# Kernel tuning notes

Hardware: AMD Instinct MI355X
Metric: run time of the kernel (lower is better)

## Reference

```python
import jax, jax.numpy as jnp
import numpy as np

HID = 257

def _lstm_cell(x, h, c, wih, whh, bih, bhh):
    # PyTorch gate order: i, f, g, o
    g = wih @ x + bih + whh @ h + bhh
    i, f, gg, o = jnp.split(g, 4)
    c2 = jax.nn.sigmoid(f) * c + jax.nn.sigmoid(i) * jnp.tanh(gg)
    h2 = jax.nn.sigmoid(o) * jnp.tanh(c2)
    return h2, c2

def _bilstm(x, state, p):
    # seq_len==1 bidirectional LSTM: fwd and bwd cells both see the single step
    hf, cf, hb, cb = state
    hf2, cf2 = _lstm_cell(x, hf, cf, p[0], p[1], p[2], p[3])
    hb2, cb2 = _lstm_cell(x, hb, cb, p[4], p[5], p[6], p[7])
    return jnp.concatenate([hf2, hb2]), (hf2, cf2, hb2, cb2)

def _conv_relu(x, w, b):
    y = jax.lax.conv_general_dilated(x, w, (1, 1), 'VALID', dimension_numbers=('NCHW', 'OIHW', 'NCHW'))
    return jax.nn.relu(y + b[None, :, None, None])

def _forward(src, conv1_w, conv1_b, conv2_w, conv2_b, conv3_w, conv3_b, conv4_w, conv4_b,
             conv5_w, conv5_b, conv6_w, conv6_b, fc1_w, fc1_b, fc2_w, fc2_b, fc3_w, fc3_b,
             enc_wih_f, enc_whh_f, enc_bih_f, enc_bhh_f, enc_wih_b, enc_whh_b, enc_bih_b, enc_bhh_b,
             dec_wih_f, dec_whh_f, dec_bih_f, dec_bhh_f, dec_wih_b, dec_whh_b, dec_bih_b, dec_bhh_b,
             lin_w, lin_b, maxlinelen):
    # AdaptiveMaxPool2d(32) on 128x128 == 4x4/stride-4 max pool
    x = src.reshape(1, 32, 32, 4, 32, 4).max(axis=(3, 5))
    x = _conv_relu(x, conv1_w, conv1_b)   # (1,64,30,30)
    x = _conv_relu(x, conv2_w, conv2_b)   # (1,128,28,28)
    x = _conv_relu(x, conv3_w, conv3_b)   # (1,256,26,26)
    x = _conv_relu(x, conv4_w, conv4_b)   # (1,512,24,24)
    x = _conv_relu(x, conv5_w, conv5_b)   # (1,512,22,22)
    x = _conv_relu(x, conv6_w, conv6_b)   # (1,512,21,21) (k=2)
    # AdaptiveMaxPool2d(10) on 21x21 == window-3/stride-2 max pool
    x = jax.lax.reduce_window(x, -jnp.inf, jax.lax.max, (1, 1, 3, 3), (1, 1, 2, 2), 'VALID')
    x = x.reshape(-1)                     # (51200,)
    x = jax.nn.relu(fc1_w @ x + fc1_b)
    x = jax.nn.relu(fc2_w @ x + fc2_b)
    feat = fc3_w @ x + fc3_b              # (128,)
    enc_p = (enc_wih_f, enc_whh_f, enc_bih_f, enc_bhh_f, enc_wih_b, enc_whh_b, enc_bih_b, enc_bhh_b)
    dec_p = (dec_wih_f, dec_whh_f, dec_bih_f, dec_bhh_f, dec_wih_b, dec_whh_b, dec_bih_b, dec_bhh_b)
    z = jnp.zeros((HID,), src.dtype)
    y, enc_state = _bilstm(feat, (z, z, z, z), enc_p)  # encode, zero init state
    x = lin_w @ y + lin_b
    y, state = _bilstm(x, enc_state, dec_p)            # decode seeded with encode hidden
    x = lin_w @ y + lin_b                              # out[0]
    def step(carry, _):
        xc, st = carry
        yy, st2 = _bilstm(xc, st, dec_p)
        x2 = lin_w @ yy + lin_b
        return (x2, st2), x2
    _, rest = jax.lax.scan(step, (x, state), None, length=maxlinelen - 1)
    return jnp.concatenate([x[None, :], rest], axis=0)  # (maxlinelen, 257)

def setup_inputs():
    key = jax.random.key(0)
    ks = iter(jax.random.split(key, 64))
    def W(shape, fan):
        return jax.random.normal(next(ks), shape, jnp.float32) / np.float32(np.sqrt(fan))
    d = {}
    d['src'] = jax.random.normal(next(ks), (1, 32, 128, 128), jnp.float32)
    convs = [(64, 32, 3), (128, 64, 3), (256, 128, 3), (512, 256, 3), (512, 512, 3), (512, 512, 2)]
    for i, (o, c, k) in enumerate(convs, 1):
        d['conv%d_w' % i] = W((o, c, k, k), c * k * k)
        d['conv%d_b' % i] = jnp.zeros((o,), jnp.float32)
    d['fc1_w'] = W((2048, 51200), 51200); d['fc1_b'] = jnp.zeros((2048,), jnp.float32)
    d['fc2_w'] = W((512, 2048), 2048);    d['fc2_b'] = jnp.zeros((512,), jnp.float32)
    d['fc3_w'] = W((128, 512), 512);      d['fc3_b'] = jnp.zeros((128,), jnp.float32)
    for pre, nin in (('enc', 128), ('dec', HID)):
        for dr in ('f', 'b'):
            d['%s_wih_%s' % (pre, dr)] = W((4 * HID, nin), HID)
            d['%s_whh_%s' % (pre, dr)] = W((4 * HID, HID), HID)
            d['%s_bih_%s' % (pre, dr)] = jnp.zeros((4 * HID,), jnp.float32)
            d['%s_bhh_%s' % (pre, dr)] = jnp.zeros((4 * HID,), jnp.float32)
    d['lin_w'] = W((HID, 2 * HID), 2 * HID)
    d['lin_b'] = jnp.zeros((HID,), jnp.float32)
    d['maxlinelen'] = 128
    return d

def reference(src, conv1_w, conv1_b, conv2_w, conv2_b, conv3_w, conv3_b, conv4_w, conv4_b,
              conv5_w, conv5_b, conv6_w, conv6_b, fc1_w, fc1_b, fc2_w, fc2_b, fc3_w, fc3_b,
              enc_wih_f, enc_whh_f, enc_bih_f, enc_bhh_f, enc_wih_b, enc_whh_b, enc_bih_b, enc_bhh_b,
              dec_wih_f, dec_whh_f, dec_bih_f, dec_bhh_f, dec_wih_b, dec_whh_b, dec_bih_b, dec_bhh_b,
              lin_w, lin_b, maxlinelen):
    return _forward(src, conv1_w, conv1_b, conv2_w, conv2_b, conv3_w, conv3_b, conv4_w, conv4_b,
                    conv5_w, conv5_b, conv6_w, conv6_b, fc1_w, fc1_b, fc2_w, fc2_b, fc3_w, fc3_b,
                    enc_wih_f, enc_whh_f, enc_bih_f, enc_bhh_f, enc_wih_b, enc_whh_b, enc_bih_b, enc_bhh_b,
                    dec_wih_f, dec_whh_f, dec_bih_f, dec_bhh_f, dec_wih_b, dec_whh_b, dec_bih_b, dec_bhh_b,
                    lin_w, lin_b, maxlinelen)
```

## Files before the change

### kernel.cpp

```cpp
#include <hip/hip_runtime.h>

#define DIV_UP(a,b) (((a)+(b)-1)/(b))
#define DEC_NWG 33
#define POISON 0xAAAAAAAAu

__device__ __forceinline__ float sigm(float x){ return 1.f/(1.f+__expf(-x)); }
__device__ __forceinline__ float tanh_f(float x){ return 1.f - 2.f/(__expf(2.f*x)+1.f); }

__device__ __forceinline__ void fma4x4(const float4 wv, const float4 xv, float acc[4][4]){
  acc[0][0] += wv.x*xv.x; acc[0][1] += wv.x*xv.y; acc[0][2] += wv.x*xv.z; acc[0][3] += wv.x*xv.w;
  acc[1][0] += wv.y*xv.x; acc[1][1] += wv.y*xv.y; acc[1][2] += wv.y*xv.z; acc[1][3] += wv.y*xv.w;
  acc[2][0] += wv.z*xv.x; acc[2][1] += wv.z*xv.y; acc[2][2] += wv.z*xv.z; acc[2][3] += wv.z*xv.w;
  acc[3][0] += wv.w*xv.x; acc[3][1] += wv.w*xv.y; acc[3][2] += wv.w*xv.z; acc[3][3] += wv.w*xv.w;
}

__global__ void k_setup(unsigned int* ydec){
  int idx = blockIdx.x*256 + threadIdx.x;
  if (idx < 128*576) ydec[576 + idx] = POISON;
}

__global__ void k_pool1(const float* __restrict__ src, float* __restrict__ out){
  int idx = blockIdx.x*256 + threadIdx.x;
  if (idx >= 32*32*32) return;
  int x = idx & 31, y = (idx>>5)&31, c = idx>>10;
  const float* p = src + ((size_t)(c*128) + y*4)*128 + x*4;
  float m = -1e30f;
  #pragma unroll
  for (int i=0;i<4;i++)
    #pragma unroll
    for (int j=0;j<4;j++) m = fmaxf(m, p[i*128+j]);
  out[idx] = m;
}

template<int KS>
__global__ __launch_bounds__(256) void k_conv_gemm(
    const float* __restrict__ in, const float* __restrict__ w,
    float* __restrict__ part,
    int Cin, int Hin, int Win, int Cout, int Hout, int Wout, int G, int kchunk)
{
  const int P = Hout*Wout;
  const int K = Cin*KS*KS;
  const int pxT = (P+63)>>6;
  int b = blockIdx.x;
  const int g = b % G; b /= G;
  const int pt = b % pxT; const int ot = b / pxT;
  const int k0 = g*kchunk;
  const int k1 = min(K, k0+kchunk);
  const int tid = threadIdx.x;
  const int tx = tid & 15, ty = tid >> 4;
  const int sp = tid & 63, sk = tid >> 6;
  int p_st = pt*64 + sp;
  bool pv = p_st < P;
  int pys = 0, pxs = 0;
  if (pv){ pys = p_st / Wout; pxs = p_st - pys*Wout; }
  __shared__ __align__(16) float Xs[16][64];
  __shared__ __align__(16) float Ws[16][68];
  float acc[4][4];
  #pragma unroll
  for (int i=0;i<4;i++)
    #pragma unroll
    for (int j=0;j<4;j++) acc[i][j]=0.f;
  for (int kb=k0; kb<k1; kb+=16){
    #pragma unroll
    for (int i=0;i<4;i++){
      int k = kb + sk + i*4;
      float v = 0.f;
      if (k < k1 && pv){
        int ic = k/(KS*KS); int t = k - ic*(KS*KS); int ky = t/KS, kx = t - ky*KS;
        v = in[((size_t)(ic*Hin) + pys+ky)*Win + (pxs+kx)];
      }
      Xs[sk+i*4][sp] = v;
    }
    #pragma unroll
    for (int i=0;i<4;i++){
      int k = kb + tx;
      int oc = ot*64 + ty + i*16;
      Ws[tx][ty+i*16] = (k < k1) ? w[(size_t)oc*K + k] : 0.f;
    }
    __syncthreads();
    #pragma unroll
    for (int kk=0;kk<16;kk++){
      float4 wv = *(const float4*)&Ws[kk][ty*4];
      float4 xv = *(const float4*)&Xs[kk][tx*4];
      fma4x4(wv, xv, acc);
    }
    __syncthreads();
  }
  float* po = part + (size_t)g*Cout*P;
  #pragma unroll
  for (int i=0;i<4;i++){
    int oc = ot*64 + ty*4 + i;
    #pragma unroll
    for (int j=0;j<4;j++){
      int p = pt*64 + tx*4 + j;
      if (p < P) po[(size_t)oc*P + p] = acc[i][j];
    }
  }
}

__global__ void k_conv_reduce(const float* __restrict__ part, const float* __restrict__ bias,
                              float* __restrict__ out, int Cout, int P, int G){
  int idx = blockIdx.x*256 + threadIdx.x;
  int total = Cout*P;
  if (idx >= total) return;
  int oc = idx / P;
  float s = bias[oc];
  for (int g=0; g<G; g++) s += part[(size_t)g*total + idx];
  out[idx] = fmaxf(s, 0.f);
}

__global__ void k_pool2(const float* __restrict__ in, float* __restrict__ out){
  int idx = blockIdx.x*256 + threadIdx.x;
  if (idx >= 51200) return;
  int x = idx % 10; int y = (idx/10)%10; int c = idx/100;
  const float* p = in + ((size_t)(c*21) + y*2)*21 + x*2;
  float m = -1e30f;
  #pragma unroll
  for (int i=0;i<3;i++)
    #pragma unroll
    for (int j=0;j<3;j++) m = fmaxf(m, p[i*21+j]);
  out[idx] = m;
}

__global__ __launch_bounds__(256) void k_fc(const float* __restrict__ w, const float* __restrict__ x,
                     const float* __restrict__ b, float* __restrict__ out, int N, int do_relu){
  int row = blockIdx.x;
  int tid = threadIdx.x;
  const float* wr = w + (size_t)row*N;
  float s = 0.f;
  for (int i = tid*4; i < N; i += 1024){
    float4 wv = *(const float4*)(wr + i);
    float4 xv = *(const float4*)(x + i);
    s += wv.x*xv.x + wv.y*xv.y + wv.z*xv.z + wv.w*xv.w;
  }
  #pragma unroll
  for (int off=32; off; off>>=1) s += __shfl_xor(s, off, 64);
  __shared__ float red[4];
  if ((tid & 63) == 0) red[tid>>6] = s;
  __syncthreads();
  if (tid == 0){
    float t = red[0]+red[1]+red[2]+red[3] + b[row];
    if (do_relu) t = fmaxf(t, 0.f);
    out[row] = t;
  }
}

__global__ __launch_bounds__(256) void k_gemm_wl(
    const float* __restrict__ wf, const float* __restrict__ wb,
    const float* __restrict__ lw, float* __restrict__ C)
{
  int b = blockIdx.x;
  int nt = b % 9; int mt = b / 9;
  int tid = threadIdx.x;
  int tx = tid&15, ty = tid>>4;
  int sp = tid&63, sk = tid>>6;
  __shared__ __align__(16) float Xs[16][64];
  __shared__ __align__(16) float Ws[16][68];
  float acc[4][4];
  #pragma unroll
  for (int i=0;i<4;i++)
    #pragma unroll
    for (int j=0;j<4;j++) acc[i][j]=0.f;
  for (int kb=0; kb<257; kb+=16){
    #pragma unroll
    for (int i=0;i<4;i++){
      int k = kb+sk+i*4;
      int col = nt*64 + sp;
      Xs[sk+i*4][sp] = (k<257 && col<514) ? lw[(size_t)k*514+col] : 0.f;
    }
    #pragma unroll
    for (int i=0;i<4;i++){
      int k = kb+tx;
      int row = mt*64 + ty + i*16;
      float v = 0.f;
      if (k<257 && row<2056)
        v = (row<1028) ? wf[(size_t)row*257+k] : wb[(size_t)(row-1028)*257+k];
      Ws[tx][ty+i*16] = v;
    }
    __syncthreads();
    #pragma unroll
    for (int kk=0;kk<16;kk++){
      float4 wv = *(const float4*)&Ws[kk][ty*4];
      float4 xv = *(const float4*)&Xs[kk][tx*4];
      fma4x4(wv, xv, acc);
    }
    __syncthreads();
  }
  #pragma unroll
  for (int i=0;i<4;i++){
    int row = mt*64 + ty*4 + i;
    #pragma unroll
    for (int j=0;j<4;j++){
      int col = nt*64 + tx*4 + j;
      if (row<2056 && col<514) C[(size_t)row*514+col] = acc[i][j];
    }
  }
}

__global__ void k_assemble(const float* __restrict__ C, const float* __restrict__ whf,
                           const float* __restrict__ whb, float* __restrict__ A){
  int idx = blockIdx.x*256+threadIdx.x;
  if (idx >= 528*4*576) return;
  int k = idx % 576;
  int g = (idx/576)&3;
  int u = idx/2304;
  float v = 0.f;
  if (u < 514 && k < 514){
    int j = (u<257)? u : u-257;
    int row = ((u<257)?0:1028) + g*257 + j;
    v = C[(size_t)row*514 + k];
    if (u<257){ if (k<257) v += whf[(size_t)(g*257+j)*257 + k]; }
    else      { if (k>=257) v += whb[(size_t)(g*257+j)*257 + (k-257)]; }
  }
  A[idx] = v;
}

__global__ void k_dvec(const float* __restrict__ wihf, const float* __restrict__ wihb,
                       const float* __restrict__ bihf, const float* __restrict__ bhhf,
                       const float* __restrict__ bihb, const float* __restrict__ bhhb,
                       const float* __restrict__ lb, float* __restrict__ dv){
  int row = blockIdx.x*4 + (threadIdx.x>>6);
  if (row >= 528*4) return;
  int u = row>>2, g = row&3;
  int lane = threadIdx.x & 63;
  float s = 0.f;
  float v = 0.f;
  if (u < 514){
    int j = (u<257)? u : u-257;
    int r = g*257+j;
    const float* wr = ((u<257)? wihf : wihb) + (size_t)r*257;
    for (int m=lane;m<257;m+=64) s += wr[m]*lb[m];
    #pragma unroll
    for (int off=32; off; off>>=1) s += __shfl_xor(s, off, 64);
    v = s + ((u<257) ? (bihf[r]+bhhf[r]) : (bihb[r]+bhhb[r]));
  }
  if (lane == 0) dv[row] = v;
}

__global__ void k_enc_gates(const float* __restrict__ wf, const float* __restrict__ wb,
                            const float* __restrict__ bihf, const float* __restrict__ bhhf,
                            const float* __restrict__ bihb, const float* __restrict__ bhhb,
                            const float* __restrict__ feat, float* __restrict__ gates){
  __shared__ float fs[128];
  int tid = threadIdx.x;
  if (tid < 128) fs[tid] = feat[tid];
  __syncthreads();
  int r = blockIdx.x*256 + tid;
  if (r >= 2056) return;
  const float* wr; float bias;
  if (r < 1028){ wr = wf + (size_t)r*128; bias = bihf[r]+bhhf[r]; }
  else { int rr = r-1028; wr = wb + (size_t)rr*128; bias = bihb[rr]+bhhb[rr]; }
  float s = bias;
  for (int m=0;m<128;m++) s += wr[m]*fs[m];
  gates[r] = s;
}

__global__ void k_enc_point(const float* __restrict__ gates, float* __restrict__ ydec0,
                            float* __restrict__ cinit){
  int u = blockIdx.x*256+threadIdx.x;
  if (u >= 528) return;
  float h = 0.f, c = 0.f;
  if (u < 514){
    int j = (u<257)? u : u-257;
    int base = (u<257)? 0 : 1028;
    float gi = gates[base + j];
    float gg = gates[base + 514 + j];
    float go = gates[base + 771 + j];
    c = sigm(gi)*tanh_f(gg);
    h = sigm(go)*tanh_f(c);
  }
  ydec0[u] = h; cinit[u] = c;
}

__global__ __launch_bounds__(256,1) void k_decode(
    const float* __restrict__ A, const float* __restrict__ dv,
    const float* __restrict__ cinit, float* __restrict__ Ydec)
{
  const int tid = threadIdx.x;
  const int u = blockIdx.x*16 + (tid>>4);
  const int q = tid & 15;
  float w[4][36];
  {
    const float* base = A + (size_t)u*4*576 + q*36;
    #pragma unroll
    for (int g=0; g<4; g++){
      #pragma unroll
      for (int i=0;i<36;i+=4){
        float4 v = *(const float4*)(base + g*576 + i);
        w[g][i]=v.x; w[g][i+1]=v.y; w[g][i+2]=v.z; w[g][i+3]=v.w;
      }
    }
  }
  const float4 dg = *(const float4*)(dv + u*4);
  float c = cinit[u];
  __shared__ __align__(16) float ys[2][576];
  for (int step=0; step<128; step++){
    float* ysb = ys[step&1];
    if (tid < 64){
      const unsigned int* rowp = (const unsigned int*)(Ydec + (size_t)step*576);
      unsigned int v[9];
      while (true){
        bool ok = true;
        #pragma unroll
        for (int j=0;j<9;j++){
          int idx = tid + j*64;
          v[j] = __hip_atomic_load(rowp + idx, __ATOMIC_RELAXED, __HIP_MEMORY_SCOPE_AGENT);
          if (idx < 528 && v[j] == POISON) ok = false;
        }
        if (__all(ok)) break;
      }
      #pragma unroll
      for (int j=0;j<9;j++){
        int idx = tid + j*64;
        ((unsigned int*)ysb)[idx] = (idx < 528) ? v[j] : 0u;
      }
    }
    __syncthreads();
    float s0=0.f, s1=0.f, s2=0.f, s3=0.f;
    const float4* yl4 = (const float4*)&ysb[q*36];
    #pragma unroll
    for (int i=0;i<9;i++){
      float4 yv = yl4[i];
      s0 += w[0][i*4]*yv.x + w[0][i*4+1]*yv.y + w[0][i*4+2]*yv.z + w[0][i*4+3]*yv.w;
      s1 += w[1][i*4]*yv.x + w[1][i*4+1]*yv.y + w[1][i*4+2]*yv.z + w[1][i*4+3]*yv.w;
      s2 += w[2][i*4]*yv.x + w[2][i*4+1]*yv.y + w[2][i*4+2]*yv.z + w[2][i*4+3]*yv.w;
      s3 += w[3][i*4]*yv.x + w[3][i*4+1]*yv.y + w[3][i*4+2]*yv.z + w[3][i*4+3]*yv.w;
    }
    #pragma unroll
    for (int off=8; off; off>>=1){
      s0 += __shfl_xor(s0, off, 64);
      s1 += __shfl_xor(s1, off, 64);
      s2 += __shfl_xor(s2, off, 64);
      s3 += __shfl_xor(s3, off, 64);
    }
    if (q == 0){
      float ci = sigm(s1+dg.y)*c + sigm(s0+dg.x)*tanh_f(s2+dg.z);
      c = ci;
      float h = sigm(s3+dg.w)*tanh_f(ci);
      __hip_atomic_store(Ydec + (size_t)(step+1)*576 + u, h,
                         __ATOMIC_RELAXED, __HIP_MEMORY_SCOPE_AGENT);
    }
  }
}

__global__ __launch_bounds__(256) void k_final(const float* __restrict__ Ydec, const float* __restrict__ lw,
                        const float* __restrict__ lb, float* __restrict__ out){
  __shared__ float ysl[514];
  int t = blockIdx.x, tid = threadIdx.x;
  for (int i=tid;i<514;i+=256) ysl[i] = Ydec[(size_t)(t+1)*576+i];
  __syncthreads();
  for (int m=tid; m<257; m+=256){
    float s = lb[m];
    const float* wr = lw + (size_t)m*514;
    for (int k=0;k<514;k++) s += wr[k]*ysl[k];
    out[t*257+m] = s;
  }
}

extern "C" void kernel_launch(void* const* d_in, const int* in_sizes, int n_in,
                              void* d_out, int out_size, void* d_ws, size_t ws_size,
                              hipStream_t stream){
  const float* src  = (const float*)d_in[0];
  const float* c1w = (const float*)d_in[1];  const float* c1b = (const float*)d_in[2];
  const float* c2w = (const float*)d_in[3];  const float* c2b = (const float*)d_in[4];
  const float* c3w = (const float*)d_in[5];  const float* c3b = (const float*)d_in[6];
  const float* c4w = (const float*)d_in[7];  const float* c4b = (const float*)d_in[8];
  const float* c5w = (const float*)d_in[9];  const float* c5b = (const float*)d_in[10];
  const float* c6w = (const float*)d_in[11]; const float* c6b = (const float*)d_in[12];
  const float* fc1w= (const float*)d_in[13]; const float* fc1b= (const float*)d_in[14];
  const float* fc2w= (const float*)d_in[15]; const float* fc2b= (const float*)d_in[16];
  const float* fc3w= (const float*)d_in[17]; const float* fc3b= (const float*)d_in[18];
  const float* ewihf=(const float*)d_in[19];
  const float* ebihf=(const float*)d_in[21]; const float* ebhhf=(const float*)d_in[22];
  const float* ewihb=(const float*)d_in[23];
  const float* ebihb=(const float*)d_in[25]; const float* ebhhb=(const float*)d_in[26];
  const float* dwihf=(const float*)d_in[27]; const float* dwhhf=(const float*)d_in[28];
  const float* dbihf=(const float*)d_in[29]; const float* dbhhf=(const float*)d_in[30];
  const float* dwihb=(const float*)d_in[31]; const float* dwhhb=(const float*)d_in[32];
  const float* dbihb=(const float*)d_in[33]; const float* dbhhb=(const float*)d_in[34];
  const float* lw  = (const float*)d_in[35]; const float* lbv = (const float*)d_in[36];
  float* out = (float*)d_out;

  float* W = (float*)d_ws;
  float* cinit = W + 0;
  float* gates = W + 528;
  float* dv    = W + 2584;
  float* A     = W + 4704;
  float* C     = W + 1221216;
  float* Ydec  = W + 2278000;
  float* part  = W + 2352304;
  float* X0    = W + 3531952;
  float* X1    = W + 3826864;
  float* xfc   = W + 4074672;
  float* f1    = W + 4125872;
  float* f2    = W + 4127920;
  float* feat  = W + 4128432;

  k_setup<<<288,256,0,stream>>>((unsigned int*)Ydec);

  k_gemm_wl<<<33*9,256,0,stream>>>(dwihf, dwihb, lw, C);
  k_assemble<<<DIV_UP(528*4*576,256),256,0,stream>>>(C, dwhhf, dwhhb, A);
  k_dvec<<<528,256,0,stream>>>(dwihf, dwihb, dbihf, dbhhf, dbihb, dbhhb, lbv, dv);

  k_pool1<<<128,256,0,stream>>>(src, X0);
  k_conv_gemm<3><<<1*15*18,256,0,stream>>>(X0, c1w, part, 32,32,32,  64,30,30, 18, 16);
  k_conv_reduce<<<DIV_UP(64*900,256),256,0,stream>>>(part, c1b, X1, 64, 900, 18);
  k_conv_gemm<3><<<2*13*9,256,0,stream>>>(X1, c2w, part, 64,30,30, 128,28,28, 9, 64);
  k_conv_reduce<<<DIV_UP(128*784,256),256,0,stream>>>(part, c2b, X0, 128, 784, 9);
  k_conv_gemm<3><<<4*11*6,256,0,stream>>>(X0, c3w, part, 128,28,28, 256,26,26, 6, 192);
  k_conv_reduce<<<DIV_UP(256*676,256),256,0,stream>>>(part, c3b, X1, 256, 676, 6);
  k_conv_gemm<3><<<8*9*4,256,0,stream>>>(X1, c4w, part, 256,26,26, 512,24,24, 4, 576);
  k_conv_reduce<<<DIV_UP(512*576,256),256,0,stream>>>(part, c4b, X0, 512, 576, 4);
  k_conv_gemm<3><<<8*8*4,256,0,stream>>>(X0, c5w, part, 512,24,24, 512,22,22, 4, 1152);
  k_conv_reduce<<<DIV_UP(512*484,256),256,0,stream>>>(part, c5b, X1, 512, 484, 4);
  k_conv_gemm<2><<<8*7*4,256,0,stream>>>(X1, c6w, part, 512,22,22, 512,21,21, 4, 512);
  k_conv_reduce<<<DIV_UP(512*441,256),256,0,stream>>>(part, c6b, X0, 512, 441, 4);
  k_pool2<<<200,256,0,stream>>>(X0, xfc);

  k_fc<<<2048,256,0,stream>>>(fc1w, xfc, fc1b, f1, 51200, 1);
  k_fc<<<512,256,0,stream>>>(fc2w, f1, fc2b, f2, 2048, 1);
  k_fc<<<128,256,0,stream>>>(fc3w, f2, fc3b, feat, 512, 0);

  k_enc_gates<<<9,256,0,stream>>>(ewihf, ewihb, ebihf, ebhhf, ebihb, ebhhb, feat, gates);
  k_enc_point<<<3,256,0,stream>>>(gates, Ydec, cinit);

  k_decode<<<DEC_NWG,256,0,stream>>>(A, dv, cinit, Ydec);

  k_final<<<128,256,0,stream>>>(Ydec, lw, lbv, out);
}
```

Baseline: 1.565 ms.

## Pipeline decoder poll loads and coalesce per-block hidden-state stores

The cross-block spin-wait in the persistent LSTM decoder now keeps three sets of atomic loads in flight in rotation, so polling latency overlaps with checking. It drops the double-buffered shared row for a single buffer plus an extra barrier. All lanes now compute the cell update, and the 16 outputs per block are staged in shared memory and published by one contiguous group of 16 threads. The extra __syncthreads per step and the more complex poll loop add overhead, and with a single buffer the next step's copy must not overwrite rows other warps are still reading; the added barrier is what prevents that.

New measurement: 1.518 ms. 1.03x faster.

```diff
diff --git a/kernel.cpp b/kernel.cpp
--- a/kernel.cpp
+++ b/kernel.cpp
@@ -272,12 +272,23 @@
   ydec0[u] = h; cinit[u] = c;
 }
 
+#define LOADSET(dst) \
+  { _Pragma("unroll") for (int j=0;j<9;j++) \
+      dst[j] = __hip_atomic_load(rowp + tid + j*64, __ATOMIC_RELAXED, __HIP_MEMORY_SCOPE_AGENT); }
+#define CHECKSET(src, okvar) \
+  { bool _ok = true; \
+    _Pragma("unroll") for (int j=0;j<9;j++){ int _i = tid + j*64; if (_i < 528 && src[j] == POISON) _ok = false; } \
+    okvar = __all(_ok); }
+#define COPYOUT(src) \
+  { _Pragma("unroll") for (int j=0;j<9;j++){ int _i = tid + j*64; ((unsigned int*)ysb)[_i] = (_i < 528) ? src[j] : 0u; } }
+
 __global__ __launch_bounds__(256,1) void k_decode(
     const float* __restrict__ A, const float* __restrict__ dv,
     const float* __restrict__ cinit, float* __restrict__ Ydec)
 {
   const int tid = threadIdx.x;
-  const int u = blockIdx.x*16 + (tid>>4);
+  const int u0 = tid>>4;
+  const int u = blockIdx.x*16 + u0;
   const int q = tid & 15;
   float w[4][36];
   {
@@ -293,26 +304,23 @@
   }
   const float4 dg = *(const float4*)(dv + u*4);
   float c = cinit[u];
-  __shared__ __align__(16) float ys[2][576];
+  __shared__ __align__(16) float ys[576];
+  __shared__ float hs[16];
   for (int step=0; step<128; step++){
-    float* ysb = ys[step&1];
+    float* ysb = ys;
     if (tid < 64){
       const unsigned int* rowp = (const unsigned int*)(Ydec + (size_t)step*576);
-      unsigned int v[9];
-      while (true){
-        bool ok = true;
-        #pragma unroll
-        for (int j=0;j<9;j++){
-          int idx = tid + j*64;
-          v[j] = __hip_atomic_load(rowp + idx, __ATOMIC_RELAXED, __HIP_MEMORY_SCOPE_AGENT);
-          if (idx < 528 && v[j] == POISON) ok = false;
-        }
-        if (__all(ok)) break;
-      }
-      #pragma unroll
-      for (int j=0;j<9;j++){
-        int idx = tid + j*64;
-        ((unsigned int*)ysb)[idx] = (idx < 528) ? v[j] : 0u;
+      unsigned int va[9], vb[9], vc[9];
+      int ok;
+      LOADSET(va);
+      LOADSET(vb);
+      for(;;){
+        LOADSET(vc);
+        CHECKSET(va, ok); if (ok){ COPYOUT(va); break; }
+        LOADSET(va);
+        CHECKSET(vb, ok); if (ok){ COPYOUT(vb); break; }
+        LOADSET(vb);
+        CHECKSET(vc, ok); if (ok){ COPYOUT(vc); break; }
       }
     }
     __syncthreads();
@@ -333,12 +341,14 @@
       s2 += __shfl_xor(s2, off, 64);
       s3 += __shfl_xor(s3, off, 64);
     }
-    if (q == 0){
-      float ci = sigm(s1+dg.y)*c + sigm(s0+dg.x)*tanh_f(s2+dg.z);
-      c = ci;
-      float h = sigm(s3+dg.w)*tanh_f(ci);
-      __hip_atomic_store(Ydec + (size_t)(step+1)*576 + u, h,
-                         __ATOMIC_RELAXED, __HIP_MEMORY_SCOPE_AGENT);
+    float ci = sigm(s1+dg.y)*c + sigm(s0+dg.x)*tanh_f(s2+dg.z);
+    c = ci;
+    float h = sigm(s3+dg.w)*tanh_f(ci);
+    if (q == 0) hs[u0] = h;
+    __syncthreads();
+    if (tid < 16){
+      __hip_atomic_store((unsigned int*)(Ydec + (size_t)(step+1)*576) + blockIdx.x*16 + tid,
+                         __float_as_uint(hs[tid]), __ATOMIC_RELAXED, __HIP_MEMORY_SCOPE_AGENT);
     }
   }
 }
```
